# Kernel tuning notes

Measured on AMD Instinct MI355X. Metric: run time of the kernel, lower is better.

Reference implementation:

```python
import jax, jax.numpy as jnp
import numpy as np

T, INPUT_DIM, HIDDEN_DIM = 4096, 512, 2048
LEAK = 0.3
SPECTRAL_RADIUS = 0.9
BIAS_SCALE = 0.0
POWER_ITERS = 20


def setup_inputs() -> dict:
    key = jax.random.key(0)
    kU, kWin, kW, kv = jax.random.split(key, 4)
    U = jax.random.normal(kU, (T, INPUT_DIM), dtype=jnp.float32)
    Win = jax.random.normal(kWin, (HIDDEN_DIM, INPUT_DIM), dtype=jnp.float32)
    W = jax.random.normal(kW, (HIDDEN_DIM, HIDDEN_DIM), dtype=jnp.float32)
    # spectral scaling via power iteration (mirrors _spectral_scale_)
    v = jax.random.normal(kv, (HIDDEN_DIM, 1), dtype=jnp.float32)
    def body(v, _):
        v = W @ v
        v = v / (jnp.linalg.norm(v) + 1e-8)
        return v, None
    v, _ = jax.lax.scan(body, v, None, length=POWER_ITERS)
    s = jnp.linalg.norm(W @ v)
    W = W * (SPECTRAL_RADIUS / s)
    bias = jnp.zeros((HIDDEN_DIM,), dtype=jnp.float32) * BIAS_SCALE
    return {"U": U, "Win": Win, "W": W, "bias": bias}


def reference(U, Win, W, bias):
    def step(h, u):
        pre = Win @ u + W @ h + bias
        h = (1.0 - LEAK) * h + LEAK * jnp.tanh(pre)
        return h, h
    h0 = jnp.zeros((W.shape[0],), dtype=U.dtype)
    _, H = jax.lax.scan(step, h0, U)  # H: (T, hidden_dim)
    return H
```

## Files before the change

kernel.cpp:

```cpp
#include <hip/hip_runtime.h>
#include <hip/hip_bf16.h>
#include <math.h>

#define T_STEPS 4096
#define IN_DIM  512
#define HID     2048
#define LEAK    0.3f

#define GBM 64
#define GBN 64
#define GBK 32

__global__ __launch_bounds__(256) void gemm_p(const float* __restrict__ U,
                                              const float* __restrict__ Win,
                                              const float* __restrict__ bias,
                                              float* __restrict__ P) {
  __shared__ float As[GBM][GBK + 1];
  __shared__ float Bs[GBN][GBK + 1];
  const int bm = blockIdx.x, bn = blockIdx.y;
  const int tid = threadIdx.x;
  const int tx = tid & 15, ty = tid >> 4;

  float acc[4][4];
#pragma unroll
  for (int m = 0; m < 4; ++m)
#pragma unroll
    for (int n = 0; n < 4; ++n) acc[m][n] = 0.f;

  const float* Ub = U + (size_t)bm * GBM * IN_DIM;
  const float* Wb = Win + (size_t)bn * GBN * IN_DIM;

  for (int k0 = 0; k0 < IN_DIM; k0 += GBK) {
#pragma unroll
    for (int v = 0; v < 2; ++v) {
      const int f4 = v * 256 + tid;
      const int row = f4 >> 3;
      const int c4 = (f4 & 7) << 2;
      const float4 a = *(const float4*)(Ub + (size_t)row * IN_DIM + k0 + c4);
      As[row][c4 + 0] = a.x; As[row][c4 + 1] = a.y;
      As[row][c4 + 2] = a.z; As[row][c4 + 3] = a.w;
      const float4 b = *(const float4*)(Wb + (size_t)row * IN_DIM + k0 + c4);
      Bs[row][c4 + 0] = b.x; Bs[row][c4 + 1] = b.y;
      Bs[row][c4 + 2] = b.z; Bs[row][c4 + 3] = b.w;
    }
    __syncthreads();
#pragma unroll 8
    for (int k = 0; k < GBK; ++k) {
      float a[4], b[4];
#pragma unroll
      for (int m = 0; m < 4; ++m) a[m] = As[ty * 4 + m][k];
#pragma unroll
      for (int n = 0; n < 4; ++n) b[n] = Bs[tx * 4 + n][k];
#pragma unroll
      for (int m = 0; m < 4; ++m)
#pragma unroll
        for (int n = 0; n < 4; ++n)
          acc[m][n] = fmaf(a[m], b[n], acc[m][n]);
    }
    __syncthreads();
  }

#pragma unroll
  for (int m = 0; m < 4; ++m) {
    const int gr = bm * GBM + ty * 4 + m;
#pragma unroll
    for (int n = 0; n < 4; ++n) {
      const int gc = bn * GBN + tx * 4 + n;
      P[(size_t)gr * HID + gc] = acc[m][n] + bias[gc];
    }
  }
}

#define NB   128
#define NT   256
#define RPB  (HID / NB)
#define TPR  16
#define NF4  (HID / (TPR * 4))
#define WPT  (HID / NT)

__device__ __forceinline__ float fast_tanh(float x) {
  const float e = __expf(2.f * x);
  return 1.f - 2.f / (e + 1.f);
}

__device__ __forceinline__ void pub(unsigned long long* p, unsigned tag, float v) {
  const unsigned long long w =
      ((unsigned long long)tag << 32) | (unsigned long long)__float_as_uint(v);
  __hip_atomic_store(p, w, __ATOMIC_RELAXED, __HIP_MEMORY_SCOPE_AGENT);
}

__global__ __launch_bounds__(NT, 1) void esn_recur(const float* __restrict__ W,
                                                   float* __restrict__ out,
                                                   unsigned long long* __restrict__ slots) {
  const int tid = threadIdx.x;
  const int j   = tid & (TPR - 1);
  const int rl  = tid >> 4;
  const int row = blockIdx.x * RPB + rl;

  __shared__ float Wl[RPB][HID];
  __shared__ float hs[2][HID];

  {
    const float4* wsrc = (const float4*)(W + (size_t)blockIdx.x * RPB * HID);
    float4* wdst = (float4*)&Wl[0][0];
#pragma unroll 4
    for (int f = tid; f < RPB * HID / 4; f += NT) wdst[f] = wsrc[f];
  }

  float hp = LEAK * fast_tanh(out[row]);
  if (j == 0) {
    pub(&slots[row], 1u, hp);
    out[row] = hp;
  }

  for (int t = 1; t < T_STEPS; ++t) {
    float* __restrict__ ocur = out + (size_t)t * HID;
    const float p = ocur[row];

    const unsigned long long* __restrict__ s8 =
        slots + (size_t)((t - 1) & 1) * HID + (size_t)tid * WPT;
    const unsigned tg = (unsigned)t;
    unsigned long long w[WPT];
    do {
      w[0] = __hip_atomic_load(&s8[0], __ATOMIC_RELAXED, __HIP_MEMORY_SCOPE_AGENT);
    } while ((unsigned)(w[0] >> 32) != tg);
    bool ok;
    do {
      ok = true;
#pragma unroll
      for (int q = 1; q < WPT; ++q)
        w[q] = __hip_atomic_load(&s8[q], __ATOMIC_RELAXED, __HIP_MEMORY_SCOPE_AGENT);
#pragma unroll
      for (int q = 1; q < WPT; ++q)
        ok = ok && ((unsigned)(w[q] >> 32) == tg);
    } while (!ok);

    float* __restrict__ hb = hs[(t - 1) & 1];
    float4 v0, v1;
    v0.x = __uint_as_float((unsigned)w[0]);
    v0.y = __uint_as_float((unsigned)w[1]);
    v0.z = __uint_as_float((unsigned)w[2]);
    v0.w = __uint_as_float((unsigned)w[3]);
    v1.x = __uint_as_float((unsigned)w[4]);
    v1.y = __uint_as_float((unsigned)w[5]);
    v1.z = __uint_as_float((unsigned)w[6]);
    v1.w = __uint_as_float((unsigned)w[7]);
    *(float4*)&hb[tid * WPT]     = v0;
    *(float4*)&hb[tid * WPT + 4] = v1;
    __syncthreads();

    const float* __restrict__ wl = &Wl[rl][0];
    float4 acc = make_float4(0.f, 0.f, 0.f, 0.f);
#pragma unroll
    for (int i = 0; i < NF4; ++i) {
      const int idx = (i * TPR + j) * 4;
      const float4 wv = *(const float4*)&wl[idx];
      const float4 hv = *(const float4*)&hb[idx];
      acc.x = fmaf(wv.x, hv.x, acc.x);
      acc.y = fmaf(wv.y, hv.y, acc.y);
      acc.z = fmaf(wv.z, hv.z, acc.z);
      acc.w = fmaf(wv.w, hv.w, acc.w);
    }
    float a = (acc.x + acc.y) + (acc.z + acc.w);
    a += __shfl_xor(a, 1, TPR);
    a += __shfl_xor(a, 2, TPR);
    a += __shfl_xor(a, 4, TPR);
    a += __shfl_xor(a, 8, TPR);

    const float h = (1.f - LEAK) * hp + LEAK * fast_tanh(p + a);
    hp = h;
    if (j == 0) {
      pub(&slots[(size_t)(t & 1) * HID + row], (unsigned)(t + 1), h);
      ocur[row] = h;
    }
  }
}

extern "C" void kernel_launch(void* const* d_in, const int* in_sizes, int n_in,
                              void* d_out, int out_size, void* d_ws, size_t ws_size,
                              hipStream_t stream) {
  const float* U    = (const float*)d_in[0];
  const float* Win  = (const float*)d_in[1];
  const float* W    = (const float*)d_in[2];
  const float* bias = (const float*)d_in[3];
  float* out = (float*)d_out;
  unsigned long long* slots = (unsigned long long*)d_ws;

  hipMemsetAsync(d_ws, 0, 2 * HID * sizeof(unsigned long long), stream);

  dim3 ggrid(T_STEPS / GBM, HID / GBN);
  gemm_p<<<ggrid, 256, 0, stream>>>(U, Win, bias, out);

  esn_recur<<<NB, NT, 0, stream>>>(W, out, slots);
}
```

Baseline: 12.06 ms.

## Run redundant recurrence block groups and take the earliest published hidden state

The persistent recurrence kernel now launches two groups of 128 blocks that each compute the full hidden state redundantly. Each group publishes into its own slot ring, which grows from two to eight entries, and consumers poll both rings and accept whichever copy arrives first. The goal is to cut the cross-block synchronisation latency that a straggling block adds at every timestep. Output stores are delayed by four steps so they do not overwrite precomputed input projections still to be read, and only group 0 writes them. The cost is doubled compute and polling traffic and a dependence on all 256 blocks being co-resident.

Measured after the change: 18.61 ms. +54.3%, slower.

```diff
diff --git a/kernel.cpp b/kernel.cpp
--- a/kernel.cpp
+++ b/kernel.cpp
@@ -71,95 +71,122 @@
   }
 }
 
-#define NB   128
+#define NB   256
+#define NGB  128
 #define NT   256
-#define RPB  (HID / NB)
+#define RPB  (HID / NGB)
 #define TPR  16
 #define NF4  (HID / (TPR * 4))
 #define WPT  (HID / NT)
+#define RING 8
+
+typedef unsigned long long ull;
 
 __device__ __forceinline__ float fast_tanh(float x) {
   const float e = __expf(2.f * x);
   return 1.f - 2.f / (e + 1.f);
 }
 
-__device__ __forceinline__ void pub(unsigned long long* p, unsigned tag, float v) {
-  const unsigned long long w =
-      ((unsigned long long)tag << 32) | (unsigned long long)__float_as_uint(v);
+__device__ __forceinline__ void pub(ull* p, unsigned tag, float v) {
+  const ull w = ((ull)tag << 32) | (ull)__float_as_uint(v);
   __hip_atomic_store(p, w, __ATOMIC_RELAXED, __HIP_MEMORY_SCOPE_AGENT);
+}
+
+__device__ __forceinline__ ull ald(const ull* p) {
+  return __hip_atomic_load(p, __ATOMIC_RELAXED, __HIP_MEMORY_SCOPE_AGENT);
 }
 
 __global__ __launch_bounds__(NT, 1) void esn_recur(const float* __restrict__ W,
                                                    float* __restrict__ out,
-                                                   unsigned long long* __restrict__ slots) {
+                                                   ull* __restrict__ slots) {
   const int tid = threadIdx.x;
   const int j   = tid & (TPR - 1);
   const int rl  = tid >> 4;
-  const int row = blockIdx.x * RPB + rl;
+  const int grp = blockIdx.x >> 7;
+  const int pb  = blockIdx.x & (NGB - 1);
+  const int row = pb * RPB + rl;
 
   __shared__ float Wl[RPB][HID];
   __shared__ float hs[2][HID];
 
   {
-    const float4* wsrc = (const float4*)(W + (size_t)blockIdx.x * RPB * HID);
+    const float4* wsrc = (const float4*)(W + (size_t)pb * RPB * HID);
     float4* wdst = (float4*)&Wl[0][0];
 #pragma unroll 4
     for (int f = tid; f < RPB * HID / 4; f += NT) wdst[f] = wsrc[f];
   }
 
-  float hp = LEAK * fast_tanh(out[row]);
-  if (j == 0) {
-    pub(&slots[row], 1u, hp);
-    out[row] = hp;
+  float hp = 0.f, g0 = 0.f, g1 = 0.f, g2 = 0.f, g3 = 0.f;
+
+  if (grp == 0) {
+    hp = LEAK * fast_tanh(out[row]);
+    if (j == 0) pub(&slots[(size_t)0 * HID + row], 1u, hp);
+    g0 = hp;
   }
 
   for (int t = 1; t < T_STEPS; ++t) {
-    float* __restrict__ ocur = out + (size_t)t * HID;
-    const float p = ocur[row];
-
-    const unsigned long long* __restrict__ s8 =
-        slots + (size_t)((t - 1) & 1) * HID + (size_t)tid * WPT;
+    if (grp == 0 && j == 0 && t >= 4)
+      out[(size_t)(t - 4) * HID + row] = g3;
+    g3 = g2; g2 = g1; g1 = g0;
+
+    const float p = out[(size_t)t * HID + row];
+
+    const ull* __restrict__ sA =
+        slots + (size_t)((t - 1) & (RING - 1)) * HID + (size_t)tid * WPT;
+    const ull* __restrict__ sB = sA + (size_t)RING * HID;
     const unsigned tg = (unsigned)t;
-    unsigned long long w[WPT];
-    do {
-      w[0] = __hip_atomic_load(&s8[0], __ATOMIC_RELAXED, __HIP_MEMORY_SCOPE_AGENT);
-    } while ((unsigned)(w[0] >> 32) != tg);
+    for (;;) {
+      ull w0 = ald(sA);
+      if ((unsigned)(w0 >> 32) == tg) break;
+      w0 = ald(sB);
+      if ((unsigned)(w0 >> 32) == tg) break;
+    }
+
+    ull wv[WPT];
     bool ok;
     do {
+      ull wa[WPT], wb[WPT];
+#pragma unroll
+      for (int q = 0; q < WPT; ++q) wa[q] = ald(sA + q);
+#pragma unroll
+      for (int q = 0; q < WPT; ++q) wb[q] = ald(sB + q);
       ok = true;
 #pragma unroll
-      for (int q = 1; q < WPT; ++q)
-        w[q] = __hip_atomic_load(&s8[q], __ATOMIC_RELAXED, __HIP_MEMORY_SCOPE_AGENT);
-#pragma unroll
-      for (int q = 1; q < WPT; ++q)
-        ok = ok && ((unsigned)(w[q] >> 32) == tg);
+      for (int q = 0; q < WPT; ++q) {
+        const bool ga = ((unsigned)(wa[q] >> 32) == tg);
+        const bool gb = ((unsigned)(wb[q] >> 32) == tg);
+        wv[q] = ga ? wa[q] : wb[q];
+        ok = ok && (ga || gb);
+      }
     } while (!ok);
 
     float* __restrict__ hb = hs[(t - 1) & 1];
     float4 v0, v1;
-    v0.x = __uint_as_float((unsigned)w[0]);
-    v0.y = __uint_as_float((unsigned)w[1]);
-    v0.z = __uint_as_float((unsigned)w[2]);
-    v0.w = __uint_as_float((unsigned)w[3]);
-    v1.x = __uint_as_float((unsigned)w[4]);
-    v1.y = __uint_as_float((unsigned)w[5]);
-    v1.z = __uint_as_float((unsigned)w[6]);
-    v1.w = __uint_as_float((unsigned)w[7]);
+    v0.x = __uint_as_float((unsigned)wv[0]);
+    v0.y = __uint_as_float((unsigned)wv[1]);
+    v0.z = __uint_as_float((unsigned)wv[2]);
+    v0.w = __uint_as_float((unsigned)wv[3]);
+    v1.x = __uint_as_float((unsigned)wv[4]);
+    v1.y = __uint_as_float((unsigned)wv[5]);
+    v1.z = __uint_as_float((unsigned)wv[6]);
+    v1.w = __uint_as_float((unsigned)wv[7]);
     *(float4*)&hb[tid * WPT]     = v0;
     *(float4*)&hb[tid * WPT + 4] = v1;
     __syncthreads();
 
+    if (grp == 1 && t == 1) hp = hb[row];
+
     const float* __restrict__ wl = &Wl[rl][0];
     float4 acc = make_float4(0.f, 0.f, 0.f, 0.f);
 #pragma unroll
     for (int i = 0; i < NF4; ++i) {
       const int idx = (i * TPR + j) * 4;
-      const float4 wv = *(const float4*)&wl[idx];
-      const float4 hv = *(const float4*)&hb[idx];
-      acc.x = fmaf(wv.x, hv.x, acc.x);
-      acc.y = fmaf(wv.y, hv.y, acc.y);
-      acc.z = fmaf(wv.z, hv.z, acc.z);
-      acc.w = fmaf(wv.w, hv.w, acc.w);
+      const float4 wvv = *(const float4*)&wl[idx];
+      const float4 hv  = *(const float4*)&hb[idx];
+      acc.x = fmaf(wvv.x, hv.x, acc.x);
+      acc.y = fmaf(wvv.y, hv.y, acc.y);
+      acc.z = fmaf(wvv.z, hv.z, acc.z);
+      acc.w = fmaf(wvv.w, hv.w, acc.w);
     }
     float a = (acc.x + acc.y) + (acc.z + acc.w);
     a += __shfl_xor(a, 1, TPR);
@@ -169,10 +196,17 @@
 
     const float h = (1.f - LEAK) * hp + LEAK * fast_tanh(p + a);
     hp = h;
-    if (j == 0) {
-      pub(&slots[(size_t)(t & 1) * HID + row], (unsigned)(t + 1), h);
-      ocur[row] = h;
-    }
+    g0 = h;
+    if (j == 0)
+      pub(&slots[(size_t)(grp * RING + (t & (RING - 1))) * HID + row],
+          (unsigned)(t + 1), h);
+  }
+
+  if (grp == 0 && j == 0) {
+    out[(size_t)(T_STEPS - 4) * HID + row] = g3;
+    out[(size_t)(T_STEPS - 3) * HID + row] = g2;
+    out[(size_t)(T_STEPS - 2) * HID + row] = g1;
+    out[(size_t)(T_STEPS - 1) * HID + row] = g0;
   }
 }
 
@@ -184,9 +218,9 @@
   const float* W    = (const float*)d_in[2];
   const float* bias = (const float*)d_in[3];
   float* out = (float*)d_out;
-  unsigned long long* slots = (unsigned long long*)d_ws;
-
-  hipMemsetAsync(d_ws, 0, 2 * HID * sizeof(unsigned long long), stream);
+  ull* slots = (ull*)d_ws;
+
+  hipMemsetAsync(d_ws, 0, (size_t)2 * RING * HID * sizeof(ull), stream);
 
   dim3 ggrid(T_STEPS / GBM, HID / GBN);
   gemm_p<<<ggrid, 256, 0, stream>>>(U, Win, bias, out);
```
